# Kernel optimization log

Measured on AMD Instinct MI355X. Metric: run time of the kernel, lower is better.

Reference implementation:

```python
import jax, jax.numpy as jnp
import numpy as np

B, S, D, H = 2, 2048, 1024, 16
HD = D // H  # 64


def setup_inputs() -> dict:
    key = jax.random.key(0)
    k1, k2, k3, k4, k5, k6 = jax.random.split(key, 6)
    x = jax.random.normal(k1, (B, S, D), dtype=jnp.float32)
    # binary mask source (1.0 = masked-out position), multiplied by -1e9 inside
    mask = (jax.random.uniform(k2, (B, S, S), dtype=jnp.float32) < 0.1).astype(jnp.float32)
    lim = 1.0 / np.sqrt(D)
    Wqkv = jax.random.uniform(k3, (D, 3 * D), dtype=jnp.float32, minval=-lim, maxval=lim)
    bqkv = jax.random.uniform(k4, (3 * D,), dtype=jnp.float32, minval=-lim, maxval=lim)
    Wo = jax.random.uniform(k5, (D, D), dtype=jnp.float32, minval=-lim, maxval=lim)
    bo = jax.random.uniform(k6, (D,), dtype=jnp.float32, minval=-lim, maxval=lim)
    return {"x": x, "mask": mask, "Wqkv": Wqkv, "bqkv": bqkv, "Wo": Wo, "bo": bo}


def reference(x, mask, Wqkv, bqkv, Wo, bo):
    b, s, d = x.shape
    qkv = x @ Wqkv + bqkv                              # [B,S,3D]
    qkv = qkv.reshape(b, s, 3, H, HD).transpose(2, 0, 3, 1, 4)  # [3,B,H,S,HD]
    q, k, v = qkv[0], qkv[1], qkv[2]
    scale = 1.0 / jnp.sqrt(jnp.float32(HD))
    scores = jnp.einsum('bhqd,bhkd->bhqk', q, k) * scale
    scores = scores + mask[:, None, :, :] * (-1e9)     # broadcast over heads
    attn = jax.nn.softmax(scores, axis=-1)             # [B,H,S,S]
    values = jnp.einsum('bhqk,bhkd->bhqd', attn, v)    # [B,H,S,HD]
    # faithful to source: permute(1,0,2,3) then reshape(B,S,H*HD)
    values = values.transpose(1, 0, 2, 3).reshape(b, s, H * HD)
    return values @ Wo + bo
```

## Files before the change

### kernel.cpp

```cpp
#include <hip/hip_runtime.h>
#include <stdint.h>

#define BB 2
#define SS 2048
#define DD 1024
#define HH 16
#define HD 64
#define BH 32
#define BS 4096

typedef short bf16x8 __attribute__((ext_vector_type(8)));
typedef float f32x4 __attribute__((ext_vector_type(4)));

static __device__ __forceinline__ unsigned short f2bf(float f) {
    union { float f; unsigned int u; } x;
    x.f = f;
    unsigned int u = x.u;
    unsigned int r = u + 0x7FFFu + ((u >> 16) & 1u);
    return (unsigned short)(r >> 16);
}

static __device__ __forceinline__ void gld16(unsigned short* lds, const unsigned short* g) {
    __builtin_amdgcn_global_load_lds(
        (const __attribute__((address_space(1))) unsigned int*)g,
        (__attribute__((address_space(3))) unsigned int*)lds,
        16, 0, 0);
}

__global__ __launch_bounds__(256) void prep(
    const float* __restrict__ x, unsigned short* __restrict__ xb,
    const float* __restrict__ Wqkv, unsigned short* __restrict__ WqkvT,
    const float* __restrict__ Wo, unsigned short* __restrict__ WoT) {
    __shared__ float tile[32][33];
    int bid = blockIdx.x;
    int tid = threadIdx.x;
    if (bid < 4096) {
        int i = (bid * 256 + tid) * 4;
        float4 v = *(const float4*)(x + i);
        ushort4 o;
        o.x = f2bf(v.x); o.y = f2bf(v.y); o.z = f2bf(v.z); o.w = f2bf(v.w);
        *(ushort4*)(xb + i) = o;
    } else {
        const float* W;
        unsigned short* WT;
        int N, t;
        if (bid < 7168) { W = Wqkv; WT = WqkvT; N = 3072; t = bid - 4096; }
        else            { W = Wo;   WT = WoT;   N = 1024; t = bid - 7168; }
        const int K = 1024;
        int nx = N >> 5;
        int n0 = (t % nx) * 32, k0 = (t / nx) * 32;
        int tx = tid & 31, ty = tid >> 5;
#pragma unroll
        for (int i = 0; i < 4; i++)
            tile[ty + i * 8][tx] = W[(size_t)(k0 + ty + i * 8) * N + n0 + tx];
        __syncthreads();
#pragma unroll
        for (int i = 0; i < 4; i++)
            WT[(size_t)(n0 + ty + i * 8) * K + k0 + tx] = f2bf(tile[tx][ty + i * 8]);
    }
}

__global__ __launch_bounds__(256) void qkv_gemm(
    const unsigned short* __restrict__ xb,
    const unsigned short* __restrict__ WqkvT,
    const float* __restrict__ bqkv,
    const float* __restrict__ mask,
    unsigned int* __restrict__ mbitsT,
    unsigned short* __restrict__ q_ws,
    unsigned short* __restrict__ k_ws,
    unsigned short* __restrict__ vB) {
    __shared__ unsigned short ldsA[4096], ldsB[4096];
    int gxr = blockIdx.x;
    int tid = threadIdx.x;
    int xcd = gxr & 7, lidx = gxr >> 3;
    int m0 = (xcd * 4 + (lidx & 3)) * 128;
    int n0 = (lidx >> 2) * 128;
    int w = tid >> 6, lane = tid & 63, quad = lane >> 4, l15 = lane & 15;
    int q4 = quad * 4;

    int r = tid >> 2, p = tid & 3;
    int c = (p - (r >> 1)) & 3;
    const unsigned short* gA0 = xb + (size_t)(m0 + r) * 1024 + c * 8;
    const unsigned short* gA1 = gA0 + (size_t)64 * 1024;
    const unsigned short* gB0 = WqkvT + (size_t)(n0 + r) * 1024 + c * 8;
    const unsigned short* gB1 = gB0 + (size_t)64 * 1024;
    unsigned short* lA0 = ldsA + w * 512;
    unsigned short* lA1 = ldsA + 2048 + w * 512;
    unsigned short* lB0 = ldsB + w * 512;
    unsigned short* lB1 = ldsB + 2048 + w * 512;

    int wm = w >> 1, wn = w & 1;
    int posq = ((quad + (l15 >> 1)) & 3) * 8;
    int aoff = (wm * 64 + l15) * 32 + posq;
    int boff = (wn * 64 + l15) * 32 + posq;

    int t = n0 >> 10;
    f32x4 acc[4][4] = {};
    if (t == 2) {
        for (int k0 = 0; k0 < 1024; k0 += 32) {
            __syncthreads();
            gld16(lA0, gA0 + k0);
            gld16(lA1, gA1 + k0);
            gld16(lB0, gB0 + k0);
            gld16(lB1, gB1 + k0);
            __syncthreads();
            bf16x8 af[4], bfr[4];
#pragma unroll
            for (int i = 0; i < 4; i++) {
                af[i]  = *(const bf16x8*)(ldsA + aoff + i * 512);
                bfr[i] = *(const bf16x8*)(ldsB + boff + i * 512);
            }
#pragma unroll
            for (int i = 0; i < 4; i++)
#pragma unroll
                for (int j = 0; j < 4; j++)
                    acc[i][j] = __builtin_amdgcn_mfma_f32_16x16x32_bf16(af[i], bfr[j], acc[i][j], 0, 0, 0);
        }
    } else {
        for (int k0 = 0; k0 < 1024; k0 += 32) {
            __syncthreads();
            gld16(lA0, gA0 + k0);
            gld16(lA1, gA1 + k0);
            gld16(lB0, gB0 + k0);
            gld16(lB1, gB1 + k0);
            __syncthreads();
            bf16x8 af[4], bfr[4];
#pragma unroll
            for (int i = 0; i < 4; i++) {
                af[i]  = *(const bf16x8*)(ldsA + aoff + i * 512);
                bfr[i] = *(const bf16x8*)(ldsB + boff + i * 512);
            }
#pragma unroll
            for (int i = 0; i < 4; i++)
#pragma unroll
                for (int j = 0; j < 4; j++)
                    acc[i][j] = __builtin_amdgcn_mfma_f32_16x16x32_bf16(bfr[j], af[i], acc[i][j], 0, 0, 0);
        }
    }

    int ncol0 = n0 + wn * 64;
    int hh = (ncol0 >> 6) & 15;

    if (t == 2) {
        int rowbase = m0 + wm * 64;
        int b = rowbase >> 11;
        int kt = (rowbase >> 6) & 31;
        int bh = b * 16 + hh;
#pragma unroll
        for (int j = 0; j < 4; j++) {
            int hd = j * 16 + l15;
            float bias = bqkv[ncol0 + hd];
#pragma unroll
            for (int i = 0; i < 4; i++) {
                unsigned short* dst = vB +
                    (((((size_t)bh * 32 + kt) * 2 + (i >> 1)) * 4 + quad) * 64 + hd) * 8 + (i & 1) * 4;
                ushort4 pk;
                pk.x = f2bf(acc[i][j][0] + bias);
                pk.y = f2bf(acc[i][j][1] + bias);
                pk.z = f2bf(acc[i][j][2] + bias);
                pk.w = f2bf(acc[i][j][3] + bias);
                *(ushort4*)dst = pk;
            }
        }
    } else {
        unsigned short* dst = (t == 0) ? q_ws : k_ws;
        int sBase = m0 + wm * 64;
#pragma unroll
        for (int j = 0; j < 4; j++) {
            float4 b4 = *(const float4*)(bqkv + ncol0 + j * 16 + q4);
#pragma unroll
            for (int i = 0; i < 4; i++) {
                int row = sBase + i * 16 + l15;
                int b = row >> 11, s = row & 2047;
                int bh = b * 16 + hh;
                ushort4 pk;
                pk.x = f2bf(acc[i][j][0] + b4.x);
                pk.y = f2bf(acc[i][j][1] + b4.y);
                pk.z = f2bf(acc[i][j][2] + b4.z);
                pk.w = f2bf(acc[i][j][3] + b4.w);
                *(ushort4*)(dst + ((size_t)(bh * 2048 + s)) * 64 + j * 16 + q4) = pk;
            }
        }
    }

    {
        int wid = gxr * 4 + w;
        for (int row = wid; row < 4096; row += 3072) {
            const float* mrow = mask + (size_t)row * 2048 + lane * 32;
            unsigned int wbits = 0;
#pragma unroll
            for (int cc = 0; cc < 8; cc++) {
                float4 v = *(const float4*)(mrow + cc * 4);
                wbits |= (v.x != 0.0f ? 1u : 0u) << (cc * 4);
                wbits |= (v.y != 0.0f ? 2u : 0u) << (cc * 4);
                wbits |= (v.z != 0.0f ? 4u : 0u) << (cc * 4);
                wbits |= (v.w != 0.0f ? 8u : 0u) << (cc * 4);
            }
            int b = row >> 11, sq = row & 2047;
            mbitsT[((size_t)b * 64 + lane) * 2048 + sq] = wbits;
        }
    }
}

__global__ __launch_bounds__(256) void out_gemm(
    const unsigned short* __restrict__ Amat,
    const unsigned short* __restrict__ WoT,
    const float* __restrict__ bo,
    float* __restrict__ out) {
    __shared__ unsigned short ldsA[4096], ldsB[2048];
    int gxr = blockIdx.x;
    int xcd = gxr & 7, lidx = gxr >> 3;
    int m0 = (xcd * 4 + (lidx & 3)) * 128;
    int n0 = (lidx >> 2) * 64;
    int tid = threadIdx.x;
    int w = tid >> 6, lane = tid & 63, quad = lane >> 4, l15 = lane & 15;
    int q4 = quad * 4;

    int r = tid >> 2, p = tid & 3;
    int c = (p - (r >> 1)) & 3;
    const unsigned short* gA0 = Amat + (size_t)(m0 + r) * 1024 + c * 8;
    const unsigned short* gA1 = gA0 + (size_t)64 * 1024;
    const unsigned short* gB0 = WoT + (size_t)(n0 + r) * 1024 + c * 8;
    unsigned short* lA0 = ldsA + w * 512;
    unsigned short* lA1 = ldsA + 2048 + w * 512;
    unsigned short* lB0 = ldsB + w * 512;

    int wm = w >> 1, wn = w & 1;
    int posq = ((quad + (l15 >> 1)) & 3) * 8;
    int aoff = (wm * 64 + l15) * 32 + posq;
    int boff = (wn * 32 + l15) * 32 + posq;

    f32x4 acc[4][2] = {};
    for (int k0 = 0; k0 < 1024; k0 += 32) {
        __syncthreads();
        gld16(lA0, gA0 + k0);
        gld16(lA1, gA1 + k0);
        gld16(lB0, gB0 + k0);
        __syncthreads();
        bf16x8 af[4], bfr[2];
#pragma unroll
        for (int i = 0; i < 4; i++) af[i] = *(const bf16x8*)(ldsA + aoff + i * 512);
#pragma unroll
        for (int j = 0; j < 2; j++) bfr[j] = *(const bf16x8*)(ldsB + boff + j * 512);
#pragma unroll
        for (int i = 0; i < 4; i++)
#pragma unroll
            for (int j = 0; j < 2; j++)
                acc[i][j] = __builtin_amdgcn_mfma_f32_16x16x32_bf16(bfr[j], af[i], acc[i][j], 0, 0, 0);
    }
    int ncol0 = n0 + wn * 32;
    int rBase = m0 + wm * 64;
#pragma unroll
    for (int j = 0; j < 2; j++) {
        float4 b4 = *(const float4*)(bo + ncol0 + j * 16 + q4);
#pragma unroll
        for (int i = 0; i < 4; i++) {
            int row = rBase + i * 16 + l15;
            float4 o4;
            o4.x = acc[i][j][0] + b4.x;
            o4.y = acc[i][j][1] + b4.y;
            o4.z = acc[i][j][2] + b4.z;
            o4.w = acc[i][j][3] + b4.w;
            *(float4*)(out + (size_t)row * 1024 + ncol0 + j * 16 + q4) = o4;
        }
    }
}

__global__ __launch_bounds__(256) void attn(
    const unsigned short* __restrict__ q_ws,
    const unsigned short* __restrict__ k_ws,
    const unsigned short* __restrict__ vB,
    const unsigned int* __restrict__ mbitsT,
    unsigned short* __restrict__ o_ws) {
    __shared__ unsigned short ldsK[8192];
    __shared__ unsigned short ldsV[8192];

    int tid = threadIdx.x;
    int w = tid >> 6, lane = tid & 63, quad = lane >> 4, l15 = lane & 15;
    int bxr = blockIdx.x;
    int bx = ((bxr & 7) << 7) | (bxr >> 3);
    int bh = bx >> 5, qt = bx & 31;
    int b = bh >> 4, h = bh & 15;

    int q = qt * 64 + w * 16 + l15;
    const unsigned short* qptr = q_ws + ((size_t)(bh * 2048 + q)) * 64 + quad * 8;
    bf16x8 qf0 = *(const bf16x8*)(qptr);
    bf16x8 qf1 = *(const bf16x8*)(qptr + 32);

    const float c2 = 0.125f * 1.44269504089f;
    const float Cs = c2 * 8388608.0f;
    const float Ds = (127.0f - 16.0f) * 8388608.0f;

    const unsigned int* mb = mbitsT + (size_t)b * 64 * 2048 + q;
    const unsigned short* kbase = k_ws + (size_t)bh * 2048 * 64;
    const unsigned short* vbb = vB + (size_t)bh * 32 * 4096;

    int srow = (lane >> 3);
    int spos = lane & 7;
    unsigned short* dK0 = ldsK + w * 1024 + lane * 8;
    unsigned short* dV0 = ldsV + w * 1024 + lane * 8;
    int r0 = w * 16 + srow;
    int r1 = r0 + 8;
    int g0 = spos ^ (r0 & 7);
    int g1 = spos ^ (r1 & 7);
    const unsigned short* kS0n = kbase + (size_t)r0 * 64 + g0 * 8;
    const unsigned short* kS1n = kbase + (size_t)r1 * 64 + g1 * 8;
    const unsigned short* vSn  = vbb + (size_t)w * 1024 + lane * 8;
    const unsigned int* mbn = mb;

    f32x4 oacc[4] = {};
    f32x4 lacc = {};
    bf16x8 onesA;
#pragma unroll
    for (int j = 0; j < 8; j++) onesA[j] = (short)0x3F80;

    int sw = (l15 & 7);
    int q4 = quad * 4;

    gld16(dK0, kS0n);
    gld16(dK0 + 512, kS1n);
    gld16(dV0, vSn);
    gld16(dV0 + 512, vSn + 512);
    kS0n += 4096; kS1n += 4096; vSn += 4096;
    unsigned int mw0 = mbn[0];
    unsigned int mw1 = mbn[2048];
    mbn += 4096;
    __syncthreads();

    unsigned int nw0, nw1;

#define ATTN_BODY(KT, CO)                                                          \
    {                                                                              \
        nw0 = 0; nw1 = 0;                                                          \
        if ((KT) < 31) {                 \
            gld16(dK0 + ((CO) ^ 4096), kS0n);                                      \
            gld16(dK0 + ((CO) ^ 4096) + 512, kS1n);                                \
            gld16(dV0 + ((CO) ^ 4096), vSn);                                       \
            gld16(dV0 + ((CO) ^ 4096) + 512, vSn + 512);                           \
            kS0n += 4096; kS1n += 4096; vSn += 4096;                               \
            nw0 = mbn[0]; nw1 = mbn[2048]; mbn += 4096;                            \
        }                                                                          \
        f32x4 sacc[4];                                                             \
        __builtin_amdgcn_s_setprio(1);                                             \
        _Pragma("unroll")                                                          \
        for (int nt = 0; nt < 4; nt++) {                                           \
            const unsigned short* kr = ldsK + (CO) + (nt * 16 + l15) * 64;         \
            bf16x8 kf0, kf1;                                                       \
            __builtin_memcpy(&kf0, kr + (quad ^ sw) * 8, 16);                      \
            __builtin_memcpy(&kf1, kr + ((quad + 4) ^ sw) * 8, 16);                \
            f32x4 z = {};                                                          \
            z = __builtin_amdgcn_mfma_f32_16x16x32_bf16(kf0, qf0, z, 0, 0, 0);     \
            z = __builtin_amdgcn_mfma_f32_16x16x32_bf16(kf1, qf1, z, 0, 0, 0);     \
            sacc[nt] = z;                                                          \
        }                                                                          \
        __builtin_amdgcn_s_setprio(0);                                             \
        unsigned int s0 = mw0 >> q4;                                               \
        unsigned int s1 = mw1 >> q4;                                               \
        unsigned int dw[4][2];                                                     \
        _Pragma("unroll")                                                          \
        for (int nt = 0; nt < 4; nt++) {                                           \
            unsigned int sel = (nt & 2) ? s1 : s0;                                 \
            unsigned int u[4];                                                     \
            _Pragma("unroll")                                                      \
            for (int rr = 0; rr < 4; rr++) {                                       \
                float y = __builtin_fmaf(sacc[nt][rr], Cs, Ds);                    \
                if ((sel >> ((nt & 1) * 16 + rr)) & 1u) y = 0.f;                   \
                u[rr] = (unsigned int)(int)y;                                      \
            }                                                                      \
            dw[nt][0] = __builtin_amdgcn_perm(u[1], u[0], 0x07060302u);            \
            dw[nt][1] = __builtin_amdgcn_perm(u[3], u[2], 0x07060302u);            \
        }                                                                          \
        __builtin_amdgcn_s_setprio(1);                                             \
        _Pragma("unroll")                                                          \
        for (int ks2 = 0; ks2 < 2; ks2++) {                                        \
            union { bf16x8 v; unsigned int d[4]; } bfr;                            \
            bfr.d[0] = dw[2 * ks2][0];                                             \
            bfr.d[1] = dw[2 * ks2][1];                                             \
            bfr.d[2] = dw[2 * ks2 + 1][0];                                         \
            bfr.d[3] = dw[2 * ks2 + 1][1];                                         \
            _Pragma("unroll")                                                      \
            for (int nb = 0; nb < 4; nb++) {                                       \
                bf16x8 vf;                                                         \
                __builtin_memcpy(&vf,                                              \
                    ldsV + (CO) + ((ks2 * 4 + quad) * 64 + nb * 16 + l15) * 8, 16);\
                oacc[nb] = __builtin_amdgcn_mfma_f32_16x16x32_bf16(vf, bfr.v,      \
                                                                   oacc[nb], 0, 0, 0); \
            }                                                                      \
            lacc = __builtin_amdgcn_mfma_f32_16x16x32_bf16(onesA, bfr.v, lacc,     \
                                                           0, 0, 0);               \
        }                                                                          \
        __builtin_amdgcn_s_setprio(0);                                             \
        __syncthreads();               \
        mw0 = nw0; mw1 = nw1;                                                      \
    }

    for (int kt = 0; kt < 32; kt += 2) {
        ATTN_BODY(kt, 0);
        ATTN_BODY(kt + 1, 4096);
    }
#undef ATTN_BODY

    float linv = 1.0f / lacc[0];
    unsigned short* base = o_ws + ((size_t)((h * 2 + b) * 2048 + q)) * 64;
#pragma unroll
    for (int nb = 0; nb < 4; nb++) {
        ushort4 pk;
        pk.x = f2bf(oacc[nb][0] * linv);
        pk.y = f2bf(oacc[nb][1] * linv);
        pk.z = f2bf(oacc[nb][2] * linv);
        pk.w = f2bf(oacc[nb][3] * linv);
        *(ushort4*)(base + nb * 16 + quad * 4) = pk;
    }
}


extern "C" void kernel_launch(void* const* d_in, const int* in_sizes, int n_in,
                              void* d_out, int out_size, void* d_ws, size_t ws_size,
                              hipStream_t stream) {
    const float* x    = (const float*)d_in[0];
    const float* mask = (const float*)d_in[1];
    const float* Wqkv = (const float*)d_in[2];
    const float* bqkv = (const float*)d_in[3];
    const float* Wo   = (const float*)d_in[4];
    const float* bo   = (const float*)d_in[5];
    float* out = (float*)d_out;

    char* ws = (char*)d_ws;
    unsigned short* xb    = (unsigned short*)(ws);
    unsigned short* WqkvT = (unsigned short*)(ws + ((size_t)8 << 20));
    unsigned short* WoT   = (unsigned short*)(ws + ((size_t)14 << 20));
    unsigned short* q_ws  = (unsigned short*)(ws + ((size_t)16 << 20));
    unsigned short* k_ws  = (unsigned short*)(ws + ((size_t)24 << 20));
    unsigned short* vB    = (unsigned short*)(ws + ((size_t)32 << 20));
    unsigned short* o_ws  = (unsigned short*)(ws + ((size_t)40 << 20));
    unsigned int*   mbits = (unsigned int*)(ws + ((size_t)48 << 20));

    prep<<<8192, 256, 0, stream>>>(x, xb, Wqkv, WqkvT, Wo, WoT);
    qkv_gemm<<<768, 256, 0, stream>>>(xb, WqkvT, bqkv, mask, mbits, q_ws, k_ws, vB);
    attn<<<1024, 256, 0, stream>>>(q_ws, k_ws, vB, mbits, o_ws);
    out_gemm<<<512, 256, 0, stream>>>(o_ws, WoT, bo, out);
}
```

Measured before the change: 221.0 us.

## Fuse all stages into one persistent cooperative kernel with grid syncs

Merges prep, QKV GEMM, mask bit-packing, attention and output GEMM into a single cooperative kernel of 1024 blocks that separates stages with grid-wide syncs, replacing four launches. Mask packing now runs on idle blocks (bid>=768) in parallel with the QKV GEMM instead of as a tail on GEMM blocks. The separate kernels stay as a fallback when the cooperative launch is unavailable. In exchange, grid.sync barriers add cost, occupancy is tied to 4 blocks per CU with a shared 32KB LDS buffer, and prep work becomes a strided loop.

```diff
diff --git a/kernel.cpp b/kernel.cpp
--- a/kernel.cpp
+++ b/kernel.cpp
@@ -1,5 +1,8 @@
 #include <hip/hip_runtime.h>
+#include <hip/hip_cooperative_groups.h>
 #include <stdint.h>
+
+namespace cg = cooperative_groups;
 
 #define BB 2
 #define SS 2048
@@ -27,165 +30,170 @@
         16, 0, 0);
 }
 
-__global__ __launch_bounds__(256) void prep(
-    const float* __restrict__ x, unsigned short* __restrict__ xb,
-    const float* __restrict__ Wqkv, unsigned short* __restrict__ WqkvT,
-    const float* __restrict__ Wo, unsigned short* __restrict__ WoT) {
-    __shared__ float tile[32][33];
+__global__ __launch_bounds__(256, 4) void fused(
+    const float* __restrict__ x, const float* __restrict__ mask,
+    const float* __restrict__ Wqkv, const float* __restrict__ bqkv,
+    const float* __restrict__ Wo, const float* __restrict__ bo,
+    float* __restrict__ out,
+    unsigned short* __restrict__ xb, unsigned short* __restrict__ WqkvT,
+    unsigned short* __restrict__ WoT, unsigned short* __restrict__ q_ws,
+    unsigned short* __restrict__ k_ws, unsigned short* __restrict__ vB,
+    unsigned short* __restrict__ o_ws, unsigned int* __restrict__ mbitsT) {
+    __shared__ unsigned short smem[16384];
+    cg::grid_group grid = cg::this_grid();
     int bid = blockIdx.x;
     int tid = threadIdx.x;
-    if (bid < 4096) {
-        int i = (bid * 256 + tid) * 4;
-        float4 v = *(const float4*)(x + i);
-        ushort4 o;
-        o.x = f2bf(v.x); o.y = f2bf(v.y); o.z = f2bf(v.z); o.w = f2bf(v.w);
-        *(ushort4*)(xb + i) = o;
-    } else {
-        const float* W;
-        unsigned short* WT;
-        int N, t;
-        if (bid < 7168) { W = Wqkv; WT = WqkvT; N = 3072; t = bid - 4096; }
-        else            { W = Wo;   WT = WoT;   N = 1024; t = bid - 7168; }
-        const int K = 1024;
-        int nx = N >> 5;
-        int n0 = (t % nx) * 32, k0 = (t / nx) * 32;
-        int tx = tid & 31, ty = tid >> 5;
-#pragma unroll
-        for (int i = 0; i < 4; i++)
-            tile[ty + i * 8][tx] = W[(size_t)(k0 + ty + i * 8) * N + n0 + tx];
-        __syncthreads();
-#pragma unroll
-        for (int i = 0; i < 4; i++)
-            WT[(size_t)(n0 + ty + i * 8) * K + k0 + tx] = f2bf(tile[tx][ty + i * 8]);
-    }
-}
-
-__global__ __launch_bounds__(256) void qkv_gemm(
-    const unsigned short* __restrict__ xb,
-    const unsigned short* __restrict__ WqkvT,
-    const float* __restrict__ bqkv,
-    const float* __restrict__ mask,
-    unsigned int* __restrict__ mbitsT,
-    unsigned short* __restrict__ q_ws,
-    unsigned short* __restrict__ k_ws,
-    unsigned short* __restrict__ vB) {
-    __shared__ unsigned short ldsA[4096], ldsB[4096];
-    int gxr = blockIdx.x;
-    int tid = threadIdx.x;
-    int xcd = gxr & 7, lidx = gxr >> 3;
-    int m0 = (xcd * 4 + (lidx & 3)) * 128;
-    int n0 = (lidx >> 2) * 128;
     int w = tid >> 6, lane = tid & 63, quad = lane >> 4, l15 = lane & 15;
     int q4 = quad * 4;
 
-    int r = tid >> 2, p = tid & 3;
-    int c = (p - (r >> 1)) & 3;
-    const unsigned short* gA0 = xb + (size_t)(m0 + r) * 1024 + c * 8;
-    const unsigned short* gA1 = gA0 + (size_t)64 * 1024;
-    const unsigned short* gB0 = WqkvT + (size_t)(n0 + r) * 1024 + c * 8;
-    const unsigned short* gB1 = gB0 + (size_t)64 * 1024;
-    unsigned short* lA0 = ldsA + w * 512;
-    unsigned short* lA1 = ldsA + 2048 + w * 512;
-    unsigned short* lB0 = ldsB + w * 512;
-    unsigned short* lB1 = ldsB + 2048 + w * 512;
-
-    int wm = w >> 1, wn = w & 1;
-    int posq = ((quad + (l15 >> 1)) & 3) * 8;
-    int aoff = (wm * 64 + l15) * 32 + posq;
-    int boff = (wn * 64 + l15) * 32 + posq;
-
-    int t = n0 >> 10;
-    f32x4 acc[4][4] = {};
-    if (t == 2) {
-        for (int k0 = 0; k0 < 1024; k0 += 32) {
-            __syncthreads();
-            gld16(lA0, gA0 + k0);
-            gld16(lA1, gA1 + k0);
-            gld16(lB0, gB0 + k0);
-            gld16(lB1, gB1 + k0);
-            __syncthreads();
-            bf16x8 af[4], bfr[4];
-#pragma unroll
-            for (int i = 0; i < 4; i++) {
-                af[i]  = *(const bf16x8*)(ldsA + aoff + i * 512);
-                bfr[i] = *(const bf16x8*)(ldsB + boff + i * 512);
-            }
-#pragma unroll
-            for (int i = 0; i < 4; i++)
-#pragma unroll
-                for (int j = 0; j < 4; j++)
-                    acc[i][j] = __builtin_amdgcn_mfma_f32_16x16x32_bf16(af[i], bfr[j], acc[i][j], 0, 0, 0);
+    {
+        float (*tile)[33] = (float(*)[33])smem;
+        for (int u = bid; u < 8192; u += 1024) {
+            if (u < 4096) {
+                int i = (u * 256 + tid) * 4;
+                float4 v = *(const float4*)(x + i);
+                ushort4 o;
+                o.x = f2bf(v.x); o.y = f2bf(v.y); o.z = f2bf(v.z); o.w = f2bf(v.w);
+                *(ushort4*)(xb + i) = o;
+            } else {
+                const float* W;
+                unsigned short* WT;
+                int N, t;
+                if (u < 7168) { W = Wqkv; WT = WqkvT; N = 3072; t = u - 4096; }
+                else          { W = Wo;   WT = WoT;   N = 1024; t = u - 7168; }
+                const int K = 1024;
+                int nx = N >> 5;
+                int n0 = (t % nx) * 32, k0 = (t / nx) * 32;
+                int tx = tid & 31, ty = tid >> 5;
+                __syncthreads();
+#pragma unroll
+                for (int i = 0; i < 4; i++)
+                    tile[ty + i * 8][tx] = W[(size_t)(k0 + ty + i * 8) * N + n0 + tx];
+                __syncthreads();
+#pragma unroll
+                for (int i = 0; i < 4; i++)
+                    WT[(size_t)(n0 + ty + i * 8) * K + k0 + tx] = f2bf(tile[tx][ty + i * 8]);
+            }
+        }
+    }
+    grid.sync();
+
+    if (bid < 768) {
+        unsigned short* ldsA = smem;
+        unsigned short* ldsB = smem + 4096;
+        int xcd = bid & 7, lidx = bid >> 3;
+        int m0 = (xcd * 4 + (lidx & 3)) * 128;
+        int n0 = (lidx >> 2) * 128;
+
+        int r = tid >> 2, p = tid & 3;
+        int c = (p - (r >> 1)) & 3;
+        const unsigned short* gA0 = xb + (size_t)(m0 + r) * 1024 + c * 8;
+        const unsigned short* gA1 = gA0 + (size_t)64 * 1024;
+        const unsigned short* gB0 = WqkvT + (size_t)(n0 + r) * 1024 + c * 8;
+        const unsigned short* gB1 = gB0 + (size_t)64 * 1024;
+        unsigned short* lA0 = ldsA + w * 512;
+        unsigned short* lA1 = ldsA + 2048 + w * 512;
+        unsigned short* lB0 = ldsB + w * 512;
+        unsigned short* lB1 = ldsB + 2048 + w * 512;
+
+        int wm = w >> 1, wn = w & 1;
+        int posq = ((quad + (l15 >> 1)) & 3) * 8;
+        int aoff = (wm * 64 + l15) * 32 + posq;
+        int boff = (wn * 64 + l15) * 32 + posq;
+
+        int t = n0 >> 10;
+        f32x4 acc[4][4] = {};
+        if (t == 2) {
+            for (int k0 = 0; k0 < 1024; k0 += 32) {
+                __syncthreads();
+                gld16(lA0, gA0 + k0);
+                gld16(lA1, gA1 + k0);
+                gld16(lB0, gB0 + k0);
+                gld16(lB1, gB1 + k0);
+                __syncthreads();
+                bf16x8 af[4], bfr[4];
+#pragma unroll
+                for (int i = 0; i < 4; i++) {
+                    af[i]  = *(const bf16x8*)(ldsA + aoff + i * 512);
+                    bfr[i] = *(const bf16x8*)(ldsB + boff + i * 512);
+                }
+#pragma unroll
+                for (int i = 0; i < 4; i++)
+#pragma unroll
+                    for (int j = 0; j < 4; j++)
+                        acc[i][j] = __builtin_amdgcn_mfma_f32_16x16x32_bf16(af[i], bfr[j], acc[i][j], 0, 0, 0);
+            }
+        } else {
+            for (int k0 = 0; k0 < 1024; k0 += 32) {
+                __syncthreads();
+                gld16(lA0, gA0 + k0);
+                gld16(lA1, gA1 + k0);
+                gld16(lB0, gB0 + k0);
+                gld16(lB1, gB1 + k0);
+                __syncthreads();
+                bf16x8 af[4], bfr[4];
+#pragma unroll
+                for (int i = 0; i < 4; i++) {
+                    af[i]  = *(const bf16x8*)(ldsA + aoff + i * 512);
+                    bfr[i] = *(const bf16x8*)(ldsB + boff + i * 512);
+                }
+#pragma unroll
+                for (int i = 0; i < 4; i++)
+#pragma unroll
+                    for (int j = 0; j < 4; j++)
+                        acc[i][j] = __builtin_amdgcn_mfma_f32_16x16x32_bf16(bfr[j], af[i], acc[i][j], 0, 0, 0);
+            }
+        }
+
+        int ncol0 = n0 + wn * 64;
+        int hh = (ncol0 >> 6) & 15;
+
+        if (t == 2) {
+            int rowbase = m0 + wm * 64;
+            int b = rowbase >> 11;
+            int kt = (rowbase >> 6) & 31;
+            int bh = b * 16 + hh;
+#pragma unroll
+            for (int j = 0; j < 4; j++) {
+                int hd = j * 16 + l15;
+                float bias = bqkv[ncol0 + hd];
+#pragma unroll
+                for (int i = 0; i < 4; i++) {
+                    unsigned short* dst = vB +
+                        (((((size_t)bh * 32 + kt) * 2 + (i >> 1)) * 4 + quad) * 64 + hd) * 8 + (i & 1) * 4;
+                    ushort4 pk;
+                    pk.x = f2bf(acc[i][j][0] + bias);
+                    pk.y = f2bf(acc[i][j][1] + bias);
+                    pk.z = f2bf(acc[i][j][2] + bias);
+                    pk.w = f2bf(acc[i][j][3] + bias);
+                    *(ushort4*)dst = pk;
+                }
+            }
+        } else {
+            unsigned short* dst = (t == 0) ? q_ws : k_ws;
+            int sBase = m0 + wm * 64;
+#pragma unroll
+            for (int j = 0; j < 4; j++) {
+                float4 b4 = *(const float4*)(bqkv + ncol0 + j * 16 + q4);
+#pragma unroll
+                for (int i = 0; i < 4; i++) {
+                    int row = sBase + i * 16 + l15;
+                    int b = row >> 11, s = row & 2047;
+                    int bh = b * 16 + hh;
+                    ushort4 pk;
+                    pk.x = f2bf(acc[i][j][0] + b4.x);
+                    pk.y = f2bf(acc[i][j][1] + b4.y);
+                    pk.z = f2bf(acc[i][j][2] + b4.z);
+                    pk.w = f2bf(acc[i][j][3] + b4.w);
+                    *(ushort4*)(dst + ((size_t)(bh * 2048 + s)) * 64 + j * 16 + q4) = pk;
+                }
+            }
         }
     } else {
-        for (int k0 = 0; k0 < 1024; k0 += 32) {
-            __syncthreads();
-            gld16(lA0, gA0 + k0);
-            gld16(lA1, gA1 + k0);
-            gld16(lB0, gB0 + k0);
-            gld16(lB1, gB1 + k0);
-            __syncthreads();
-            bf16x8 af[4], bfr[4];
-#pragma unroll
-            for (int i = 0; i < 4; i++) {
-                af[i]  = *(const bf16x8*)(ldsA + aoff + i * 512);
-                bfr[i] = *(const bf16x8*)(ldsB + boff + i * 512);
-            }
-#pragma unroll
-            for (int i = 0; i < 4; i++)
-#pragma unroll
-                for (int j = 0; j < 4; j++)
-                    acc[i][j] = __builtin_amdgcn_mfma_f32_16x16x32_bf16(bfr[j], af[i], acc[i][j], 0, 0, 0);
-        }
-    }
-
-    int ncol0 = n0 + wn * 64;
-    int hh = (ncol0 >> 6) & 15;
-
-    if (t == 2) {
-        int rowbase = m0 + wm * 64;
-        int b = rowbase >> 11;
-        int kt = (rowbase >> 6) & 31;
-        int bh = b * 16 + hh;
-#pragma unroll
-        for (int j = 0; j < 4; j++) {
-            int hd = j * 16 + l15;
-            float bias = bqkv[ncol0 + hd];
-#pragma unroll
-            for (int i = 0; i < 4; i++) {
-                unsigned short* dst = vB +
-                    (((((size_t)bh * 32 + kt) * 2 + (i >> 1)) * 4 + quad) * 64 + hd) * 8 + (i & 1) * 4;
-                ushort4 pk;
-                pk.x = f2bf(acc[i][j][0] + bias);
-                pk.y = f2bf(acc[i][j][1] + bias);
-                pk.z = f2bf(acc[i][j][2] + bias);
-                pk.w = f2bf(acc[i][j][3] + bias);
-                *(ushort4*)dst = pk;
-            }
-        }
-    } else {
-        unsigned short* dst = (t == 0) ? q_ws : k_ws;
-        int sBase = m0 + wm * 64;
-#pragma unroll
-        for (int j = 0; j < 4; j++) {
-            float4 b4 = *(const float4*)(bqkv + ncol0 + j * 16 + q4);
-#pragma unroll
-            for (int i = 0; i < 4; i++) {
-                int row = sBase + i * 16 + l15;
-                int b = row >> 11, s = row & 2047;
-                int bh = b * 16 + hh;
-                ushort4 pk;
-                pk.x = f2bf(acc[i][j][0] + b4.x);
-                pk.y = f2bf(acc[i][j][1] + b4.y);
-                pk.z = f2bf(acc[i][j][2] + b4.z);
-                pk.w = f2bf(acc[i][j][3] + b4.w);
-                *(ushort4*)(dst + ((size_t)(bh * 2048 + s)) * 64 + j * 16 + q4) = pk;
-            }
-        }
-    }
-
-    {
-        int wid = gxr * 4 + w;
-        for (int row = wid; row < 4096; row += 3072) {
+        int wid = (bid - 768) * 4 + w;
+#pragma unroll
+        for (int rr = 0; rr < 4; rr++) {
+            int row = wid * 4 + rr;
             const float* mrow = mask + (size_t)row * 2048 + lane * 32;
             unsigned int wbits = 0;
 #pragma unroll
@@ -200,139 +208,68 @@
             mbitsT[((size_t)b * 64 + lane) * 2048 + sq] = wbits;
         }
     }
-}
-
-__global__ __launch_bounds__(256) void out_gemm(
-    const unsigned short* __restrict__ Amat,
-    const unsigned short* __restrict__ WoT,
-    const float* __restrict__ bo,
-    float* __restrict__ out) {
-    __shared__ unsigned short ldsA[4096], ldsB[2048];
-    int gxr = blockIdx.x;
-    int xcd = gxr & 7, lidx = gxr >> 3;
-    int m0 = (xcd * 4 + (lidx & 3)) * 128;
-    int n0 = (lidx >> 2) * 64;
-    int tid = threadIdx.x;
-    int w = tid >> 6, lane = tid & 63, quad = lane >> 4, l15 = lane & 15;
-    int q4 = quad * 4;
-
-    int r = tid >> 2, p = tid & 3;
-    int c = (p - (r >> 1)) & 3;
-    const unsigned short* gA0 = Amat + (size_t)(m0 + r) * 1024 + c * 8;
-    const unsigned short* gA1 = gA0 + (size_t)64 * 1024;
-    const unsigned short* gB0 = WoT + (size_t)(n0 + r) * 1024 + c * 8;
-    unsigned short* lA0 = ldsA + w * 512;
-    unsigned short* lA1 = ldsA + 2048 + w * 512;
-    unsigned short* lB0 = ldsB + w * 512;
-
-    int wm = w >> 1, wn = w & 1;
-    int posq = ((quad + (l15 >> 1)) & 3) * 8;
-    int aoff = (wm * 64 + l15) * 32 + posq;
-    int boff = (wn * 32 + l15) * 32 + posq;
-
-    f32x4 acc[4][2] = {};
-    for (int k0 = 0; k0 < 1024; k0 += 32) {
+    grid.sync();
+
+    {
+        unsigned short* ldsK = smem;
+        unsigned short* ldsV = smem + 8192;
+
+        int bxr = bid;
+        int bx = ((bxr & 7) << 7) | (bxr >> 3);
+        int bh = bx >> 5, qt = bx & 31;
+        int b = bh >> 4, h = bh & 15;
+
+        int q = qt * 64 + w * 16 + l15;
+        const unsigned short* qptr = q_ws + ((size_t)(bh * 2048 + q)) * 64 + quad * 8;
+        bf16x8 qf0 = *(const bf16x8*)(qptr);
+        bf16x8 qf1 = *(const bf16x8*)(qptr + 32);
+
+        const float c2 = 0.125f * 1.44269504089f;
+        const float Cs = c2 * 8388608.0f;
+        const float Ds = (127.0f - 16.0f) * 8388608.0f;
+
+        const unsigned int* mb = mbitsT + (size_t)b * 64 * 2048 + q;
+        const unsigned short* kbase = k_ws + (size_t)bh * 2048 * 64;
+        const unsigned short* vbb = vB + (size_t)bh * 32 * 4096;
+
+        int srow = (lane >> 3);
+        int spos = lane & 7;
+        unsigned short* dK0 = ldsK + w * 1024 + lane * 8;
+        unsigned short* dV0 = ldsV + w * 1024 + lane * 8;
+        int r0 = w * 16 + srow;
+        int r1 = r0 + 8;
+        int g0 = spos ^ (r0 & 7);
+        int g1 = spos ^ (r1 & 7);
+        const unsigned short* kS0n = kbase + (size_t)r0 * 64 + g0 * 8;
+        const unsigned short* kS1n = kbase + (size_t)r1 * 64 + g1 * 8;
+        const unsigned short* vSn  = vbb + (size_t)w * 1024 + lane * 8;
+        const unsigned int* mbn = mb;
+
+        f32x4 oacc[4] = {};
+        f32x4 lacc = {};
+        bf16x8 onesA;
+#pragma unroll
+        for (int j = 0; j < 8; j++) onesA[j] = (short)0x3F80;
+
+        int sw = (l15 & 7);
+
         __syncthreads();
-        gld16(lA0, gA0 + k0);
-        gld16(lA1, gA1 + k0);
-        gld16(lB0, gB0 + k0);
+        gld16(dK0, kS0n);
+        gld16(dK0 + 512, kS1n);
+        gld16(dV0, vSn);
+        gld16(dV0 + 512, vSn + 512);
+        kS0n += 4096; kS1n += 4096; vSn += 4096;
+        unsigned int mw0 = mbn[0];
+        unsigned int mw1 = mbn[2048];
+        mbn += 4096;
         __syncthreads();
-        bf16x8 af[4], bfr[2];
-#pragma unroll
-        for (int i = 0; i < 4; i++) af[i] = *(const bf16x8*)(ldsA + aoff + i * 512);
-#pragma unroll
-        for (int j = 0; j < 2; j++) bfr[j] = *(const bf16x8*)(ldsB + boff + j * 512);
-#pragma unroll
-        for (int i = 0; i < 4; i++)
-#pragma unroll
-            for (int j = 0; j < 2; j++)
-                acc[i][j] = __builtin_amdgcn_mfma_f32_16x16x32_bf16(bfr[j], af[i], acc[i][j], 0, 0, 0);
-    }
-    int ncol0 = n0 + wn * 32;
-    int rBase = m0 + wm * 64;
-#pragma unroll
-    for (int j = 0; j < 2; j++) {
-        float4 b4 = *(const float4*)(bo + ncol0 + j * 16 + q4);
-#pragma unroll
-        for (int i = 0; i < 4; i++) {
-            int row = rBase + i * 16 + l15;
-            float4 o4;
-            o4.x = acc[i][j][0] + b4.x;
-            o4.y = acc[i][j][1] + b4.y;
-            o4.z = acc[i][j][2] + b4.z;
-            o4.w = acc[i][j][3] + b4.w;
-            *(float4*)(out + (size_t)row * 1024 + ncol0 + j * 16 + q4) = o4;
-        }
-    }
-}
-
-__global__ __launch_bounds__(256) void attn(
-    const unsigned short* __restrict__ q_ws,
-    const unsigned short* __restrict__ k_ws,
-    const unsigned short* __restrict__ vB,
-    const unsigned int* __restrict__ mbitsT,
-    unsigned short* __restrict__ o_ws) {
-    __shared__ unsigned short ldsK[8192];
-    __shared__ unsigned short ldsV[8192];
-
-    int tid = threadIdx.x;
-    int w = tid >> 6, lane = tid & 63, quad = lane >> 4, l15 = lane & 15;
-    int bxr = blockIdx.x;
-    int bx = ((bxr & 7) << 7) | (bxr >> 3);
-    int bh = bx >> 5, qt = bx & 31;
-    int b = bh >> 4, h = bh & 15;
-
-    int q = qt * 64 + w * 16 + l15;
-    const unsigned short* qptr = q_ws + ((size_t)(bh * 2048 + q)) * 64 + quad * 8;
-    bf16x8 qf0 = *(const bf16x8*)(qptr);
-    bf16x8 qf1 = *(const bf16x8*)(qptr + 32);
-
-    const float c2 = 0.125f * 1.44269504089f;
-    const float Cs = c2 * 8388608.0f;
-    const float Ds = (127.0f - 16.0f) * 8388608.0f;
-
-    const unsigned int* mb = mbitsT + (size_t)b * 64 * 2048 + q;
-    const unsigned short* kbase = k_ws + (size_t)bh * 2048 * 64;
-    const unsigned short* vbb = vB + (size_t)bh * 32 * 4096;
-
-    int srow = (lane >> 3);
-    int spos = lane & 7;
-    unsigned short* dK0 = ldsK + w * 1024 + lane * 8;
-    unsigned short* dV0 = ldsV + w * 1024 + lane * 8;
-    int r0 = w * 16 + srow;
-    int r1 = r0 + 8;
-    int g0 = spos ^ (r0 & 7);
-    int g1 = spos ^ (r1 & 7);
-    const unsigned short* kS0n = kbase + (size_t)r0 * 64 + g0 * 8;
-    const unsigned short* kS1n = kbase + (size_t)r1 * 64 + g1 * 8;
-    const unsigned short* vSn  = vbb + (size_t)w * 1024 + lane * 8;
-    const unsigned int* mbn = mb;
-
-    f32x4 oacc[4] = {};
-    f32x4 lacc = {};
-    bf16x8 onesA;
-#pragma unroll
-    for (int j = 0; j < 8; j++) onesA[j] = (short)0x3F80;
-
-    int sw = (l15 & 7);
-    int q4 = quad * 4;
-
-    gld16(dK0, kS0n);
-    gld16(dK0 + 512, kS1n);
-    gld16(dV0, vSn);
-    gld16(dV0 + 512, vSn + 512);
-    kS0n += 4096; kS1n += 4096; vSn += 4096;
-    unsigned int mw0 = mbn[0];
-    unsigned int mw1 = mbn[2048];
-    mbn += 4096;
-    __syncthreads();
-
-    unsigned int nw0, nw1;
+
+        unsigned int nw0, nw1;
 
 #define ATTN_BODY(KT, CO)                                                          \
     {                                                                              \
         nw0 = 0; nw1 = 0;                                                          \
-        if ((KT) < 31) {                 \
+        if ((KT) < 31) {                                                           \
             gld16(dK0 + ((CO) ^ 4096), kS0n);                                      \
             gld16(dK0 + ((CO) ^ 4096) + 512, kS1n);                                \
             gld16(dV0 + ((CO) ^ 4096), vSn);                                       \
@@ -390,7 +327,454 @@
                                                            0, 0, 0);               \
         }                                                                          \
         __builtin_amdgcn_s_setprio(0);                                             \
-        __syncthreads();               \
+        __syncthreads();                                                           \
+        mw0 = nw0; mw1 = nw1;                                                      \
+    }
+
+        for (int kt = 0; kt < 32; kt += 2) {
+            ATTN_BODY(kt, 0);
+            ATTN_BODY(kt + 1, 4096);
+        }
+#undef ATTN_BODY
+
+        float linv = 1.0f / lacc[0];
+        unsigned short* base = o_ws + ((size_t)((h * 2 + b) * 2048 + q)) * 64;
+#pragma unroll
+        for (int nb = 0; nb < 4; nb++) {
+            ushort4 pk;
+            pk.x = f2bf(oacc[nb][0] * linv);
+            pk.y = f2bf(oacc[nb][1] * linv);
+            pk.z = f2bf(oacc[nb][2] * linv);
+            pk.w = f2bf(oacc[nb][3] * linv);
+            *(ushort4*)(base + nb * 16 + quad * 4) = pk;
+        }
+    }
+    grid.sync();
+
+    if (bid < 512) {
+        unsigned short* ldsA = smem;
+        unsigned short* ldsB = smem + 4096;
+        int xcd = bid & 7, lidx = bid >> 3;
+        int m0 = (xcd * 4 + (lidx & 3)) * 128;
+        int n0 = (lidx >> 2) * 64;
+
+        int r = tid >> 2, p = tid & 3;
+        int c = (p - (r >> 1)) & 3;
+        const unsigned short* gA0 = o_ws + (size_t)(m0 + r) * 1024 + c * 8;
+        const unsigned short* gA1 = gA0 + (size_t)64 * 1024;
+        const unsigned short* gB0 = WoT + (size_t)(n0 + r) * 1024 + c * 8;
+        unsigned short* lA0 = ldsA + w * 512;
+        unsigned short* lA1 = ldsA + 2048 + w * 512;
+        unsigned short* lB0 = ldsB + w * 512;
+
+        int wm = w >> 1, wn = w & 1;
+        int posq = ((quad + (l15 >> 1)) & 3) * 8;
+        int aoff = (wm * 64 + l15) * 32 + posq;
+        int boff = (wn * 32 + l15) * 32 + posq;
+
+        f32x4 acc[4][2] = {};
+        __syncthreads();
+        for (int k0 = 0; k0 < 1024; k0 += 32) {
+            __syncthreads();
+            gld16(lA0, gA0 + k0);
+            gld16(lA1, gA1 + k0);
+            gld16(lB0, gB0 + k0);
+            __syncthreads();
+            bf16x8 af[4], bfr[2];
+#pragma unroll
+            for (int i = 0; i < 4; i++) af[i] = *(const bf16x8*)(ldsA + aoff + i * 512);
+#pragma unroll
+            for (int j = 0; j < 2; j++) bfr[j] = *(const bf16x8*)(ldsB + boff + j * 512);
+#pragma unroll
+            for (int i = 0; i < 4; i++)
+#pragma unroll
+                for (int j = 0; j < 2; j++)
+                    acc[i][j] = __builtin_amdgcn_mfma_f32_16x16x32_bf16(bfr[j], af[i], acc[i][j], 0, 0, 0);
+        }
+        int ncol0 = n0 + wn * 32;
+        int rBase = m0 + wm * 64;
+#pragma unroll
+        for (int j = 0; j < 2; j++) {
+            float4 b4 = *(const float4*)(bo + ncol0 + j * 16 + q4);
+#pragma unroll
+            for (int i = 0; i < 4; i++) {
+                int row = rBase + i * 16 + l15;
+                float4 o4;
+                o4.x = acc[i][j][0] + b4.x;
+                o4.y = acc[i][j][1] + b4.y;
+                o4.z = acc[i][j][2] + b4.z;
+                o4.w = acc[i][j][3] + b4.w;
+                *(float4*)(out + (size_t)row * 1024 + ncol0 + j * 16 + q4) = o4;
+            }
+        }
+    }
+}
+
+
+__global__ __launch_bounds__(256) void prep(
+    const float* __restrict__ x, unsigned short* __restrict__ xb,
+    const float* __restrict__ Wqkv, unsigned short* __restrict__ WqkvT,
+    const float* __restrict__ Wo, unsigned short* __restrict__ WoT) {
+    __shared__ float tile[32][33];
+    int bid = blockIdx.x;
+    int tid = threadIdx.x;
+    if (bid < 4096) {
+        int i = (bid * 256 + tid) * 4;
+        float4 v = *(const float4*)(x + i);
+        ushort4 o;
+        o.x = f2bf(v.x); o.y = f2bf(v.y); o.z = f2bf(v.z); o.w = f2bf(v.w);
+        *(ushort4*)(xb + i) = o;
+    } else {
+        const float* W;
+        unsigned short* WT;
+        int N, t;
+        if (bid < 7168) { W = Wqkv; WT = WqkvT; N = 3072; t = bid - 4096; }
+        else            { W = Wo;   WT = WoT;   N = 1024; t = bid - 7168; }
+        const int K = 1024;
+        int nx = N >> 5;
+        int n0 = (t % nx) * 32, k0 = (t / nx) * 32;
+        int tx = tid & 31, ty = tid >> 5;
+#pragma unroll
+        for (int i = 0; i < 4; i++)
+            tile[ty + i * 8][tx] = W[(size_t)(k0 + ty + i * 8) * N + n0 + tx];
+        __syncthreads();
+#pragma unroll
+        for (int i = 0; i < 4; i++)
+            WT[(size_t)(n0 + ty + i * 8) * K + k0 + tx] = f2bf(tile[tx][ty + i * 8]);
+    }
+}
+
+__global__ __launch_bounds__(256) void qkv_gemm(
+    const unsigned short* __restrict__ xb,
+    const unsigned short* __restrict__ WqkvT,
+    const float* __restrict__ bqkv,
+    const float* __restrict__ mask,
+    unsigned int* __restrict__ mbitsT,
+    unsigned short* __restrict__ q_ws,
+    unsigned short* __restrict__ k_ws,
+    unsigned short* __restrict__ vB) {
+    __shared__ unsigned short ldsA[4096], ldsB[4096];
+    int gxr = blockIdx.x;
+    int tid = threadIdx.x;
+    int xcd = gxr & 7, lidx = gxr >> 3;
+    int m0 = (xcd * 4 + (lidx & 3)) * 128;
+    int n0 = (lidx >> 2) * 128;
+    int w = tid >> 6, lane = tid & 63, quad = lane >> 4, l15 = lane & 15;
+    int q4 = quad * 4;
+
+    int r = tid >> 2, p = tid & 3;
+    int c = (p - (r >> 1)) & 3;
+    const unsigned short* gA0 = xb + (size_t)(m0 + r) * 1024 + c * 8;
+    const unsigned short* gA1 = gA0 + (size_t)64 * 1024;
+    const unsigned short* gB0 = WqkvT + (size_t)(n0 + r) * 1024 + c * 8;
+    const unsigned short* gB1 = gB0 + (size_t)64 * 1024;
+    unsigned short* lA0 = ldsA + w * 512;
+    unsigned short* lA1 = ldsA + 2048 + w * 512;
+    unsigned short* lB0 = ldsB + w * 512;
+    unsigned short* lB1 = ldsB + 2048 + w * 512;
+
+    int wm = w >> 1, wn = w & 1;
+    int posq = ((quad + (l15 >> 1)) & 3) * 8;
+    int aoff = (wm * 64 + l15) * 32 + posq;
+    int boff = (wn * 64 + l15) * 32 + posq;
+
+    int t = n0 >> 10;
+    f32x4 acc[4][4] = {};
+    if (t == 2) {
+        for (int k0 = 0; k0 < 1024; k0 += 32) {
+            __syncthreads();
+            gld16(lA0, gA0 + k0);
+            gld16(lA1, gA1 + k0);
+            gld16(lB0, gB0 + k0);
+            gld16(lB1, gB1 + k0);
+            __syncthreads();
+            bf16x8 af[4], bfr[4];
+#pragma unroll
+            for (int i = 0; i < 4; i++) {
+                af[i]  = *(const bf16x8*)(ldsA + aoff + i * 512);
+                bfr[i] = *(const bf16x8*)(ldsB + boff + i * 512);
+            }
+#pragma unroll
+            for (int i = 0; i < 4; i++)
+#pragma unroll
+                for (int j = 0; j < 4; j++)
+                    acc[i][j] = __builtin_amdgcn_mfma_f32_16x16x32_bf16(af[i], bfr[j], acc[i][j], 0, 0, 0);
+        }
+    } else {
+        for (int k0 = 0; k0 < 1024; k0 += 32) {
+            __syncthreads();
+            gld16(lA0, gA0 + k0);
+            gld16(lA1, gA1 + k0);
+            gld16(lB0, gB0 + k0);
+            gld16(lB1, gB1 + k0);
+            __syncthreads();
+            bf16x8 af[4], bfr[4];
+#pragma unroll
+            for (int i = 0; i < 4; i++) {
+                af[i]  = *(const bf16x8*)(ldsA + aoff + i * 512);
+                bfr[i] = *(const bf16x8*)(ldsB + boff + i * 512);
+            }
+#pragma unroll
+            for (int i = 0; i < 4; i++)
+#pragma unroll
+                for (int j = 0; j < 4; j++)
+                    acc[i][j] = __builtin_amdgcn_mfma_f32_16x16x32_bf16(bfr[j], af[i], acc[i][j], 0, 0, 0);
+        }
+    }
+
+    int ncol0 = n0 + wn * 64;
+    int hh = (ncol0 >> 6) & 15;
+
+    if (t == 2) {
+        int rowbase = m0 + wm * 64;
+        int b = rowbase >> 11;
+        int kt = (rowbase >> 6) & 31;
+        int bh = b * 16 + hh;
+#pragma unroll
+        for (int j = 0; j < 4; j++) {
+            int hd = j * 16 + l15;
+            float bias = bqkv[ncol0 + hd];
+#pragma unroll
+            for (int i = 0; i < 4; i++) {
+                unsigned short* dst = vB +
+                    (((((size_t)bh * 32 + kt) * 2 + (i >> 1)) * 4 + quad) * 64 + hd) * 8 + (i & 1) * 4;
+                ushort4 pk;
+                pk.x = f2bf(acc[i][j][0] + bias);
+                pk.y = f2bf(acc[i][j][1] + bias);
+                pk.z = f2bf(acc[i][j][2] + bias);
+                pk.w = f2bf(acc[i][j][3] + bias);
+                *(ushort4*)dst = pk;
+            }
+        }
+    } else {
+        unsigned short* dst = (t == 0) ? q_ws : k_ws;
+        int sBase = m0 + wm * 64;
+#pragma unroll
+        for (int j = 0; j < 4; j++) {
+            float4 b4 = *(const float4*)(bqkv + ncol0 + j * 16 + q4);
+#pragma unroll
+            for (int i = 0; i < 4; i++) {
+                int row = sBase + i * 16 + l15;
+                int b = row >> 11, s = row & 2047;
+                int bh = b * 16 + hh;
+                ushort4 pk;
+                pk.x = f2bf(acc[i][j][0] + b4.x);
+                pk.y = f2bf(acc[i][j][1] + b4.y);
+                pk.z = f2bf(acc[i][j][2] + b4.z);
+                pk.w = f2bf(acc[i][j][3] + b4.w);
+                *(ushort4*)(dst + ((size_t)(bh * 2048 + s)) * 64 + j * 16 + q4) = pk;
+            }
+        }
+    }
+
+    {
+        int wid = gxr * 4 + w;
+        for (int row = wid; row < 4096; row += 3072) {
+            const float* mrow = mask + (size_t)row * 2048 + lane * 32;
+            unsigned int wbits = 0;
+#pragma unroll
+            for (int cc = 0; cc < 8; cc++) {
+                float4 v = *(const float4*)(mrow + cc * 4);
+                wbits |= (v.x != 0.0f ? 1u : 0u) << (cc * 4);
+                wbits |= (v.y != 0.0f ? 2u : 0u) << (cc * 4);
+                wbits |= (v.z != 0.0f ? 4u : 0u) << (cc * 4);
+                wbits |= (v.w != 0.0f ? 8u : 0u) << (cc * 4);
+            }
+            int b = row >> 11, sq = row & 2047;
+            mbitsT[((size_t)b * 64 + lane) * 2048 + sq] = wbits;
+        }
+    }
+}
+
+__global__ __launch_bounds__(256) void out_gemm(
+    const unsigned short* __restrict__ Amat,
+    const unsigned short* __restrict__ WoT,
+    const float* __restrict__ bo,
+    float* __restrict__ out) {
+    __shared__ unsigned short ldsA[4096], ldsB[2048];
+    int gxr = blockIdx.x;
+    int xcd = gxr & 7, lidx = gxr >> 3;
+    int m0 = (xcd * 4 + (lidx & 3)) * 128;
+    int n0 = (lidx >> 2) * 64;
+    int tid = threadIdx.x;
+    int w = tid >> 6, lane = tid & 63, quad = lane >> 4, l15 = lane & 15;
+    int q4 = quad * 4;
+
+    int r = tid >> 2, p = tid & 3;
+    int c = (p - (r >> 1)) & 3;
+    const unsigned short* gA0 = Amat + (size_t)(m0 + r) * 1024 + c * 8;
+    const unsigned short* gA1 = gA0 + (size_t)64 * 1024;
+    const unsigned short* gB0 = WoT + (size_t)(n0 + r) * 1024 + c * 8;
+    unsigned short* lA0 = ldsA + w * 512;
+    unsigned short* lA1 = ldsA + 2048 + w * 512;
+    unsigned short* lB0 = ldsB + w * 512;
+
+    int wm = w >> 1, wn = w & 1;
+    int posq = ((quad + (l15 >> 1)) & 3) * 8;
+    int aoff = (wm * 64 + l15) * 32 + posq;
+    int boff = (wn * 32 + l15) * 32 + posq;
+
+    f32x4 acc[4][2] = {};
+    for (int k0 = 0; k0 < 1024; k0 += 32) {
+        __syncthreads();
+        gld16(lA0, gA0 + k0);
+        gld16(lA1, gA1 + k0);
+        gld16(lB0, gB0 + k0);
+        __syncthreads();
+        bf16x8 af[4], bfr[2];
+#pragma unroll
+        for (int i = 0; i < 4; i++) af[i] = *(const bf16x8*)(ldsA + aoff + i * 512);
+#pragma unroll
+        for (int j = 0; j < 2; j++) bfr[j] = *(const bf16x8*)(ldsB + boff + j * 512);
+#pragma unroll
+        for (int i = 0; i < 4; i++)
+#pragma unroll
+            for (int j = 0; j < 2; j++)
+                acc[i][j] = __builtin_amdgcn_mfma_f32_16x16x32_bf16(bfr[j], af[i], acc[i][j], 0, 0, 0);
+    }
+    int ncol0 = n0 + wn * 32;
+    int rBase = m0 + wm * 64;
+#pragma unroll
+    for (int j = 0; j < 2; j++) {
+        float4 b4 = *(const float4*)(bo + ncol0 + j * 16 + q4);
+#pragma unroll
+        for (int i = 0; i < 4; i++) {
+            int row = rBase + i * 16 + l15;
+            float4 o4;
+            o4.x = acc[i][j][0] + b4.x;
+            o4.y = acc[i][j][1] + b4.y;
+            o4.z = acc[i][j][2] + b4.z;
+            o4.w = acc[i][j][3] + b4.w;
+            *(float4*)(out + (size_t)row * 1024 + ncol0 + j * 16 + q4) = o4;
+        }
+    }
+}
+
+__global__ __launch_bounds__(256) void attn(
+    const unsigned short* __restrict__ q_ws,
+    const unsigned short* __restrict__ k_ws,
+    const unsigned short* __restrict__ vB,
+    const unsigned int* __restrict__ mbitsT,
+    unsigned short* __restrict__ o_ws) {
+    __shared__ unsigned short ldsK[8192];
+    __shared__ unsigned short ldsV[8192];
+
+    int tid = threadIdx.x;
+    int w = tid >> 6, lane = tid & 63, quad = lane >> 4, l15 = lane & 15;
+    int bxr = blockIdx.x;
+    int bx = ((bxr & 7) << 7) | (bxr >> 3);
+    int bh = bx >> 5, qt = bx & 31;
+    int b = bh >> 4, h = bh & 15;
+
+    int q = qt * 64 + w * 16 + l15;
+    const unsigned short* qptr = q_ws + ((size_t)(bh * 2048 + q)) * 64 + quad * 8;
+    bf16x8 qf0 = *(const bf16x8*)(qptr);
+    bf16x8 qf1 = *(const bf16x8*)(qptr + 32);
+
+    const float c2 = 0.125f * 1.44269504089f;
+    const float Cs = c2 * 8388608.0f;
+    const float Ds = (127.0f - 16.0f) * 8388608.0f;
+
+    const unsigned int* mb = mbitsT + (size_t)b * 64 * 2048 + q;
+    const unsigned short* kbase = k_ws + (size_t)bh * 2048 * 64;
+    const unsigned short* vbb = vB + (size_t)bh * 32 * 4096;
+
+    int srow = (lane >> 3);
+    int spos = lane & 7;
+    unsigned short* dK0 = ldsK + w * 1024 + lane * 8;
+    unsigned short* dV0 = ldsV + w * 1024 + lane * 8;
+    int r0 = w * 16 + srow;
+    int r1 = r0 + 8;
+    int g0 = spos ^ (r0 & 7);
+    int g1 = spos ^ (r1 & 7);
+    const unsigned short* kS0n = kbase + (size_t)r0 * 64 + g0 * 8;
+    const unsigned short* kS1n = kbase + (size_t)r1 * 64 + g1 * 8;
+    const unsigned short* vSn  = vbb + (size_t)w * 1024 + lane * 8;
+    const unsigned int* mbn = mb;
+
+    f32x4 oacc[4] = {};
+    f32x4 lacc = {};
+    bf16x8 onesA;
+#pragma unroll
+    for (int j = 0; j < 8; j++) onesA[j] = (short)0x3F80;
+
+    int sw = (l15 & 7);
+    int q4 = quad * 4;
+
+    gld16(dK0, kS0n);
+    gld16(dK0 + 512, kS1n);
+    gld16(dV0, vSn);
+    gld16(dV0 + 512, vSn + 512);
+    kS0n += 4096; kS1n += 4096; vSn += 4096;
+    unsigned int mw0 = mbn[0];
+    unsigned int mw1 = mbn[2048];
+    mbn += 4096;
+    __syncthreads();
+
+    unsigned int nw0, nw1;
+
+#define ATTN_BODY(KT, CO)                                                          \
+    {                                                                              \
+        nw0 = 0; nw1 = 0;                                                          \
+        if ((KT) < 31) {                                                           \
+            gld16(dK0 + ((CO) ^ 4096), kS0n);                                      \
+            gld16(dK0 + ((CO) ^ 4096) + 512, kS1n);                                \
+            gld16(dV0 + ((CO) ^ 4096), vSn);                                       \
+            gld16(dV0 + ((CO) ^ 4096) + 512, vSn + 512);                           \
+            kS0n += 4096; kS1n += 4096; vSn += 4096;                               \
+            nw0 = mbn[0]; nw1 = mbn[2048]; mbn += 4096;                            \
+        }                                                                          \
+        f32x4 sacc[4];                                                             \
+        __builtin_amdgcn_s_setprio(1);                                             \
+        _Pragma("unroll")                                                          \
+        for (int nt = 0; nt < 4; nt++) {                                           \
+            const unsigned short* kr = ldsK + (CO) + (nt * 16 + l15) * 64;         \
+            bf16x8 kf0, kf1;                                                       \
+            __builtin_memcpy(&kf0, kr + (quad ^ sw) * 8, 16);                      \
+            __builtin_memcpy(&kf1, kr + ((quad + 4) ^ sw) * 8, 16);                \
+            f32x4 z = {};                                                          \
+            z = __builtin_amdgcn_mfma_f32_16x16x32_bf16(kf0, qf0, z, 0, 0, 0);     \
+            z = __builtin_amdgcn_mfma_f32_16x16x32_bf16(kf1, qf1, z, 0, 0, 0);     \
+            sacc[nt] = z;                                                          \
+        }                                                                          \
+        __builtin_amdgcn_s_setprio(0);                                             \
+        unsigned int s0 = mw0 >> q4;                                               \
+        unsigned int s1 = mw1 >> q4;                                               \
+        unsigned int dw[4][2];                                                     \
+        _Pragma("unroll")                                                          \
+        for (int nt = 0; nt < 4; nt++) {                                           \
+            unsigned int sel = (nt & 2) ? s1 : s0;                                 \
+            unsigned int u[4];                                                     \
+            _Pragma("unroll")                                                      \
+            for (int rr = 0; rr < 4; rr++) {                                       \
+                float y = __builtin_fmaf(sacc[nt][rr], Cs, Ds);                    \
+                if ((sel >> ((nt & 1) * 16 + rr)) & 1u) y = 0.f;                   \
+                u[rr] = (unsigned int)(int)y;                                      \
+            }                                                                      \
+            dw[nt][0] = __builtin_amdgcn_perm(u[1], u[0], 0x07060302u);            \
+            dw[nt][1] = __builtin_amdgcn_perm(u[3], u[2], 0x07060302u);            \
+        }                                                                          \
+        __builtin_amdgcn_s_setprio(1);                                             \
+        _Pragma("unroll")                                                          \
+        for (int ks2 = 0; ks2 < 2; ks2++) {                                        \
+            union { bf16x8 v; unsigned int d[4]; } bfr;                            \
+            bfr.d[0] = dw[2 * ks2][0];                                             \
+            bfr.d[1] = dw[2 * ks2][1];                                             \
+            bfr.d[2] = dw[2 * ks2 + 1][0];                                         \
+            bfr.d[3] = dw[2 * ks2 + 1][1];                                         \
+            _Pragma("unroll")                                                      \
+            for (int nb = 0; nb < 4; nb++) {                                       \
+                bf16x8 vf;                                                         \
+                __builtin_memcpy(&vf,                                              \
+                    ldsV + (CO) + ((ks2 * 4 + quad) * 64 + nb * 16 + l15) * 8, 16);\
+                oacc[nb] = __builtin_amdgcn_mfma_f32_16x16x32_bf16(vf, bfr.v,      \
+                                                                   oacc[nb], 0, 0, 0); \
+            }                                                                      \
+            lacc = __builtin_amdgcn_mfma_f32_16x16x32_bf16(onesA, bfr.v, lacc,     \
+                                                           0, 0, 0);               \
+        }                                                                          \
+        __builtin_amdgcn_s_setprio(0);                                             \
+        __syncthreads();                                                           \
         mw0 = nw0; mw1 = nw1;                                                      \
     }
 
@@ -435,6 +819,22 @@
     unsigned short* o_ws  = (unsigned short*)(ws + ((size_t)40 << 20));
     unsigned int*   mbits = (unsigned int*)(ws + ((size_t)48 << 20));
 
+    int nb = 0;
+    hipError_t qe = hipOccupancyMaxActiveBlocksPerMultiprocessor(
+        &nb, (const void*)fused, 256, 0);
+    bool coop_ok = (qe == hipSuccess && nb >= 4);
+
+    if (coop_ok) {
+        void* args[] = { (void*)&x, (void*)&mask, (void*)&Wqkv, (void*)&bqkv,
+                         (void*)&Wo, (void*)&bo, (void*)&out,
+                         (void*)&xb, (void*)&WqkvT, (void*)&WoT, (void*)&q_ws,
+                         (void*)&k_ws, (void*)&vB, (void*)&o_ws, (void*)&mbits };
+        hipError_t le = hipLaunchCooperativeKernel(
+            (const void*)fused, dim3(1024), dim3(256), args, 0, stream);
+        if (le == hipSuccess) return;
+        (void)hipGetLastError();
+    }
+
     prep<<<8192, 256, 0, stream>>>(x, xb, Wqkv, WqkvT, Wo, WoT);
     qkv_gemm<<<768, 256, 0, stream>>>(xb, WqkvT, bqkv, mask, mbits, q_ws, k_ws, vB);
     attn<<<1024, 256, 0, stream>>>(q_ws, k_ws, vB, mbits, o_ws);
```

Result: no change. 223.0 us (+0.9%).
